# Kernel tuning notes

Measured on AMD Instinct MI355X. Metric: run time of the kernel, lower is better.

Reference implementation:

```python
import jax, jax.numpy as jnp
import numpy as np

B, N, OBS, H, S, A, K = 65536, 10, 64, 50, 10, 2, 2  # batch, agents, obs_dim, hidden, comm symbols, actions, k_steps
NEG = -1e9


def setup_inputs() -> dict:
    key = jax.random.key(0)
    ks = jax.random.split(key, 12)
    def lin(k, fan_in, shape):
        return (jax.random.uniform(k, shape, jnp.float32, -1.0, 1.0) / np.sqrt(fan_in).astype(np.float32))
    IN_F = H + S + H  # hidden + comm + skip(h0) = 110
    return {
        "obs": jax.random.normal(ks[0], (B, N, OBS), jnp.float32),
        "mask": jnp.ones((B, N), jnp.float32),
        "W_enc": lin(ks[1], OBS, (OBS, H)),
        "b_enc": lin(ks[2], OBS, (H,)),
        "W_f": lin(ks[3], IN_F, (K, IN_F, H)),
        "b_f": lin(ks[4], IN_F, (K, H)),
        "W_comm": lin(ks[5], H, (H, S)),
        "b_comm": lin(ks[6], H, (S,)),
        "W_pi": lin(ks[7], H, (H, A)),
        "b_pi": lin(ks[8], H, (A,)),
        "W_v": lin(ks[9], H, (H, 1)),
        "b_v": lin(ks[10], H, (1,)),
    }


def reference(obs, mask, W_enc, b_enc, W_f, b_f, W_comm, b_comm, W_pi, b_pi, W_v, b_v):
    mask3 = mask[..., None]                      # [B,N,1]
    h0 = jnp.tanh(obs @ W_enc + b_enc)           # [B,N,H]
    h = h0
    comm_logp = jnp.zeros(obs.shape[:2], obs.dtype)  # [B,N]
    c = jnp.zeros((*obs.shape[:2], S), obs.dtype)
    for i in range(K):  # k_steps is small & static
        comm_logits = h @ W_comm + b_comm        # [B,N,S]
        masked = jnp.where(mask3 == 0, NEG, comm_logits)
        logp = jax.nn.log_softmax(masked, axis=-1)
        w = jnp.argmax(masked, axis=-1)          # greedy symbol per agent [B,N]
        comm_logp = comm_logp + jnp.take_along_axis(logp, w[..., None], axis=-1)[..., 0] * mask
        w_onehot = jax.nn.one_hot(w, S, dtype=obs.dtype)  # [B,N,S]
        # bag-of-words OR aggregation across agents, broadcast back to every agent
        c = jnp.clip(jnp.sum(w_onehot, axis=1, keepdims=True), 0.0, 1.0)  # [B,1,S]
        c = jnp.broadcast_to(c, w_onehot.shape)  # [B,N,S]
        inp = jnp.concatenate([h, c, h0], axis=-1)  # [B,N,H+S+H]
        h = jnp.tanh(inp @ W_f[i] + b_f[i])
    logits = h @ W_pi + b_pi                      # [B,N,A]
    logits = jnp.where(mask3 == 0, NEG, logits)
    baseline = (h @ W_v + b_v)[..., 0] * mask     # [B,N]
    return logits, baseline, comm_logp, c
```

## Files before the change

### kernel.cpp

```cpp
#include <hip/hip_runtime.h>
#include <math.h>

#define NAGENT 10
#define OBS_D  64
#define HID    50
#define NSYM   10
#define NACT   2
#define KSTEPS 2
#define NEGV   (-1e9f)
#define INF    (HID + NSYM + HID)

#define BPB 6
#define TPB 64
#define AG  (BPB * NAGENT)

#define WENC_LD 52
#define WF_LD   52

#define SM_H1  (AG*51)
#define SM_C   (2*AG*51)
#define SM_TOT (SM_C + BPB*NSYM + 16)

__device__ __forceinline__ float fast_tanh(float x) {
  float xc = fminf(15.f, fmaxf(-15.f, x));
  float e  = __expf(2.f * xc);
  return __fdividef(e - 1.f, e + 1.f);
}

__global__ void prep_weights(const float* __restrict__ W_enc,
                             const float* __restrict__ W_f,
                             float* __restrict__ ws) {
  int i = blockIdx.x * blockDim.x + threadIdx.x;
  const int nEnc = OBS_D * WENC_LD;
  const int nF   = KSTEPS * INF * WF_LD;
  if (i < nEnc) {
    int k = i / WENC_LD, j = i % WENC_LD;
    ws[i] = (j < HID) ? W_enc[k*HID + j] : 0.f;
  } else if (i < nEnc + nF) {
    int r = i - nEnc;
    int s = r / (INF*WF_LD);
    int rem = r % (INF*WF_LD);
    int k = rem / WF_LD, j = rem % WF_LD;
    ws[i] = (j < HID) ? W_f[(s*INF + k)*HID + j] : 0.f;
  }
}

__global__ __launch_bounds__(TPB) void policy_kernel(
    const float* __restrict__ obs,
    const float* __restrict__ mask,
    const float* __restrict__ b_enc,
    const float* __restrict__ b_f,
    const float* __restrict__ W_comm,
    const float* __restrict__ b_comm,
    const float* __restrict__ W_pi,
    const float* __restrict__ b_pi,
    const float* __restrict__ W_v,
    const float* __restrict__ b_v,
    const float* __restrict__ W_encP,
    const float* __restrict__ W_fP,
    float* __restrict__ out,
    int B)
{
  __shared__ float smem[SM_TOT];
  const int t   = threadIdx.x;
  const int be0 = blockIdx.x * BPB;
  const int nbe = min(BPB, B - be0);
  const int nag = nbe * NAGENT;
  const int g0  = be0 * NAGENT;
  const bool act = (t < nag);
  const int ta  = act ? t : 0;
  const int bel = act ? (t / NAGENT) : 0;
  const long long g = (long long)g0 + t;
  const long long NA = (long long)B * NAGENT;

  {
    const float4* o4 = (const float4*)(obs + (long long)g0 * OBS_D);
    const int n4 = nag * (OBS_D/4);
    for (int idx = t; idx < n4; idx += TPB) {
      float4 v = o4[idx];
      int a = idx >> 4;
      int k = (idx & 15) << 2;
      float* p = &smem[a*65 + k];
      p[0]=v.x; p[1]=v.y; p[2]=v.z; p[3]=v.w;
    }
  }
  __syncthreads();

  float acc[HID];
  #pragma unroll
  for (int j=0;j<HID;j++) acc[j] = b_enc[j];
  {
    const int a65 = ta * 65;
    #pragma unroll 4
    for (int k=0;k<OBS_D;k++){
      float x = smem[a65 + k];
      const float* wr = &W_encP[k*WENC_LD];
      #pragma unroll
      for (int j=0;j<HID;j++) acc[j] = fmaf(x, wr[j], acc[j]);
    }
  }
  float hr[HID];
  #pragma unroll
  for (int j=0;j<HID;j++) hr[j] = fast_tanh(acc[j]);
  __syncthreads();
  if (act){
    #pragma unroll
    for (int j=0;j<HID;j++) smem[t*51 + j] = hr[j];
  }

  const float mk = act ? mask[g] : 1.f;
  float clp = 0.f;
  float c_reg[NSYM];

  #pragma unroll
  for (int i=0;i<KSTEPS;i++){
    float cl[NSYM];
    #pragma unroll
    for (int s=0;s<NSYM;s++) cl[s] = b_comm[s];
    #pragma unroll
    for (int k=0;k<HID;k++){
      #pragma unroll
      for (int s=0;s<NSYM;s++) cl[s] = fmaf(hr[k], W_comm[k*NSYM+s], cl[s]);
    }
    if (mk == 0.f){
      #pragma unroll
      for (int s=0;s<NSYM;s++) cl[s] = NEGV;
    }
    int w = 0; float best = cl[0];
    #pragma unroll
    for (int s=1;s<NSYM;s++){ if (cl[s] > best){ best = cl[s]; w = s; } }
    float se = 0.f;
    #pragma unroll
    for (int s=0;s<NSYM;s++) se += __expf(cl[s] - best);
    clp += (-__logf(se)) * mk;

    if (t < BPB*NSYM) smem[SM_C + t] = 0.f;
    __syncthreads();
    if (act) smem[SM_C + bel*NSYM + w] = 1.0f;
    __syncthreads();
    #pragma unroll
    for (int s=0;s<NSYM;s++) c_reg[s] = smem[SM_C + bel*NSYM + s];

    #pragma unroll
    for (int j=0;j<HID;j++) acc[j] = b_f[i*HID + j];
    #pragma unroll
    for (int s=0;s<NSYM;s++){
      const float cv = c_reg[s];
      const float* wr = &W_fP[(i*INF + HID + s)*WF_LD];
      #pragma unroll
      for (int j=0;j<HID;j++) acc[j] = fmaf(cv, wr[j], acc[j]);
    }
    const int a51 = ta*51;
    if (i == 0){
      #pragma unroll 2
      for (int k=0;k<HID;k++){
        float x = smem[a51 + k];
        const float* wa = &W_fP[(k)*WF_LD];
        const float* wd = &W_fP[(HID + NSYM + k)*WF_LD];
        #pragma unroll
        for (int j=0;j<HID;j++) acc[j] = fmaf(x, wa[j], acc[j]);
        #pragma unroll
        for (int j=0;j<HID;j++) acc[j] = fmaf(x, wd[j], acc[j]);
      }
    } else {
      #pragma unroll 2
      for (int k=0;k<HID;k++){
        float xa = smem[SM_H1 + a51 + k];
        float xd = smem[a51 + k];
        const float* wa = &W_fP[(INF + k)*WF_LD];
        const float* wd = &W_fP[(INF + HID + NSYM + k)*WF_LD];
        #pragma unroll
        for (int j=0;j<HID;j++) acc[j] = fmaf(xa, wa[j], acc[j]);
        #pragma unroll
        for (int j=0;j<HID;j++) acc[j] = fmaf(xd, wd[j], acc[j]);
      }
    }
    #pragma unroll
    for (int j=0;j<HID;j++) hr[j] = fast_tanh(acc[j]);
    if (i == 0){
      if (act){
        #pragma unroll
        for (int j=0;j<HID;j++) smem[SM_H1 + t*51 + j] = hr[j];
      }
    }
  }

  float l0 = b_pi[0], l1 = b_pi[1], bv = b_v[0];
  #pragma unroll
  for (int k=0;k<HID;k++){
    l0 = fmaf(hr[k], W_pi[k*NACT+0], l0);
    l1 = fmaf(hr[k], W_pi[k*NACT+1], l1);
    bv = fmaf(hr[k], W_v[k], bv);
  }
  if (act){
    const float lo0 = (mk==0.f) ? NEGV : l0;
    const float lo1 = (mk==0.f) ? NEGV : l1;
    out[g*2    ] = lo0;
    out[g*2 + 1] = lo1;
    out[NA*2 + g] = bv * mk;
    out[NA*3 + g] = clp;
    #pragma unroll
    for (int s=0;s<NSYM;s++) out[NA*4 + g*NSYM + s] = c_reg[s];
  }
}

extern "C" void kernel_launch(void* const* d_in, const int* in_sizes, int n_in,
                              void* d_out, int out_size, void* d_ws, size_t ws_size,
                              hipStream_t stream) {
  const float* obs    = (const float*)d_in[0];
  const float* mask   = (const float*)d_in[1];
  const float* W_enc  = (const float*)d_in[2];
  const float* b_enc  = (const float*)d_in[3];
  const float* W_f    = (const float*)d_in[4];
  const float* b_f    = (const float*)d_in[5];
  const float* W_comm = (const float*)d_in[6];
  const float* b_comm = (const float*)d_in[7];
  const float* W_pi   = (const float*)d_in[8];
  const float* b_pi   = (const float*)d_in[9];
  const float* W_v    = (const float*)d_in[10];
  const float* b_v    = (const float*)d_in[11];
  float* out = (float*)d_out;
  float* ws  = (float*)d_ws;

  const int B  = in_sizes[0] / (NAGENT * OBS_D);
  const int nP = OBS_D*WENC_LD + KSTEPS*INF*WF_LD;

  hipLaunchKernelGGL(prep_weights, dim3((nP + 255)/256), dim3(256), 0, stream,
                     W_enc, W_f, ws);

  const int grid = (B + BPB - 1) / BPB;
  hipLaunchKernelGGL(policy_kernel, dim3(grid), dim3(TPB), 0, stream,
                     obs, mask, b_enc, b_f, W_comm, b_comm, W_pi, b_pi, W_v, b_v,
                     ws, ws + OBS_D*WENC_LD, out, B);
}
```

Before: 614.7 us.

## Fold shared-input weights, replace LDS bag-of-words with ballot, stream obs directly

On step 0 h and h0 are the same vector, so the prep kernel sums their two weight blocks into one. The step-1 contribution of h0 is also computed during step 0, which lets the kernel read h0 only once. The OR aggregation across agents now uses wavefront ballots instead of shared-memory writes plus two barriers, and obs is read straight from global memory as float4 rather than staged through LDS. Outputs are written as float2, and a launch_bounds occupancy hint is added. In exchange, the pre1 accumulator array is kept live during step 0, which raises register pressure.

```diff
diff --git a/kernel.cpp b/kernel.cpp
--- a/kernel.cpp
+++ b/kernel.cpp
@@ -6,20 +6,20 @@
 #define HID    50
 #define NSYM   10
 #define NACT   2
-#define KSTEPS 2
 #define NEGV   (-1e9f)
-#define INF    (HID + NSYM + HID)
 
 #define BPB 6
 #define TPB 64
 #define AG  (BPB * NAGENT)
 
-#define WENC_LD 52
-#define WF_LD   52
-
-#define SM_H1  (AG*51)
-#define SM_C   (2*AG*51)
-#define SM_TOT (SM_C + BPB*NSYM + 16)
+#define LD 52
+
+#define OFF_WC0  3328
+#define OFF_W1S  5928
+#define OFF_W1H  8528
+#define OFF_WC0c 11128
+#define OFF_W1c  11648
+#define NPREP    (234 * LD)
 
 __device__ __forceinline__ float fast_tanh(float x) {
   float xc = fminf(15.f, fmaxf(-15.f, x));
@@ -31,21 +31,35 @@
                              const float* __restrict__ W_f,
                              float* __restrict__ ws) {
   int i = blockIdx.x * blockDim.x + threadIdx.x;
-  const int nEnc = OBS_D * WENC_LD;
-  const int nF   = KSTEPS * INF * WF_LD;
-  if (i < nEnc) {
-    int k = i / WENC_LD, j = i % WENC_LD;
-    ws[i] = (j < HID) ? W_enc[k*HID + j] : 0.f;
-  } else if (i < nEnc + nF) {
-    int r = i - nEnc;
-    int s = r / (INF*WF_LD);
-    int rem = r % (INF*WF_LD);
-    int k = rem / WF_LD, j = rem % WF_LD;
-    ws[i] = (j < HID) ? W_f[(s*INF + k)*HID + j] : 0.f;
-  }
-}
-
-__global__ __launch_bounds__(TPB) void policy_kernel(
+  if (i >= NPREP) return;
+  int j = i % LD;
+  int r = i / LD;
+  float v = 0.f;
+  if (j < HID) {
+    if      (r <  64)                { v = W_enc[r*HID + j]; }
+    else if (r < 114) { int k=r-64;    v = W_f[k*HID + j] + W_f[(60+k)*HID + j]; }
+    else if (r < 164) { int k=r-114;   v = W_f[(110+60+k)*HID + j]; }
+    else if (r < 214) { int k=r-164;   v = W_f[(110+k)*HID + j]; }
+    else if (r < 224) { int s=r-214;   v = W_f[(50+s)*HID + j]; }
+    else              { int s=r-224;   v = W_f[(110+50+s)*HID + j]; }
+  }
+  ws[i] = v;
+}
+
+__device__ __forceinline__ int comm_pick(float cl[NSYM], float mk, float& clp) {
+  #pragma unroll
+  for (int s = 0; s < NSYM; s++) cl[s] = (mk == 0.f) ? NEGV : cl[s];
+  int w = 0; float best = cl[0];
+  #pragma unroll
+  for (int s = 1; s < NSYM; s++) { bool b = cl[s] > best; best = b ? cl[s] : best; w = b ? s : w; }
+  float se = 0.f;
+  #pragma unroll
+  for (int s = 0; s < NSYM; s++) se += __expf(cl[s] - best);
+  clp += (-__logf(se)) * mk;
+  return w;
+}
+
+__global__ __launch_bounds__(TPB, 4) void policy_kernel(
     const float* __restrict__ obs,
     const float* __restrict__ mask,
     const float* __restrict__ b_enc,
@@ -56,151 +70,161 @@
     const float* __restrict__ b_pi,
     const float* __restrict__ W_v,
     const float* __restrict__ b_v,
-    const float* __restrict__ W_encP,
-    const float* __restrict__ W_fP,
+    const float* __restrict__ wsP,
     float* __restrict__ out,
     int B)
 {
-  __shared__ float smem[SM_TOT];
+  __shared__ float hbuf[AG * 51];
   const int t   = threadIdx.x;
   const int be0 = blockIdx.x * BPB;
   const int nbe = min(BPB, B - be0);
   const int nag = nbe * NAGENT;
-  const int g0  = be0 * NAGENT;
   const bool act = (t < nag);
-  const int ta  = act ? t : 0;
-  const int bel = act ? (t / NAGENT) : 0;
-  const long long g = (long long)g0 + t;
+  const int bel = t / NAGENT;
   const long long NA = (long long)B * NAGENT;
-
+  const long long g  = (long long)be0 * NAGENT + t;
+  const long long gc = act ? g : (NA - 1);
+  const int sl = act ? t : 0;
+
+  const float* WencP = wsP;
+  const float* WC0   = wsP + OFF_WC0;
+  const float* W1S   = wsP + OFF_W1S;
+  const float* W1H   = wsP + OFF_W1H;
+  const float* WC0c  = wsP + OFF_WC0c;
+  const float* W1c   = wsP + OFF_W1c;
+
+  const float mk = mask[gc];
+
+  float acc[HID];
+  #pragma unroll
+  for (int j = 0; j < HID; j++) acc[j] = b_enc[j];
   {
-    const float4* o4 = (const float4*)(obs + (long long)g0 * OBS_D);
-    const int n4 = nag * (OBS_D/4);
-    for (int idx = t; idx < n4; idx += TPB) {
-      float4 v = o4[idx];
-      int a = idx >> 4;
-      int k = (idx & 15) << 2;
-      float* p = &smem[a*65 + k];
-      p[0]=v.x; p[1]=v.y; p[2]=v.z; p[3]=v.w;
-    }
-  }
-  __syncthreads();
-
-  float acc[HID];
-  #pragma unroll
-  for (int j=0;j<HID;j++) acc[j] = b_enc[j];
+    const float4* o4 = (const float4*)(obs + gc * OBS_D);
+    #pragma unroll 2
+    for (int k4 = 0; k4 < OBS_D / 4; k4++) {
+      float4 v = o4[k4];
+      const float* wr = &WencP[k4 * 4 * LD];
+      #pragma unroll
+      for (int j = 0; j < HID; j++) acc[j] = fmaf(v.x, wr[j], acc[j]);
+      #pragma unroll
+      for (int j = 0; j < HID; j++) acc[j] = fmaf(v.y, wr[LD + j], acc[j]);
+      #pragma unroll
+      for (int j = 0; j < HID; j++) acc[j] = fmaf(v.z, wr[2 * LD + j], acc[j]);
+      #pragma unroll
+      for (int j = 0; j < HID; j++) acc[j] = fmaf(v.w, wr[3 * LD + j], acc[j]);
+    }
+  }
+
+  float cl[NSYM];
+  #pragma unroll
+  for (int s = 0; s < NSYM; s++) cl[s] = b_comm[s];
+  if (act) {
+    float* myh = &hbuf[t * 51];
+    #pragma unroll
+    for (int j = 0; j < HID; j++) {
+      float h = fast_tanh(acc[j]);
+      myh[j] = h;
+      const float* wc = &W_comm[j * NSYM];
+      #pragma unroll
+      for (int s = 0; s < NSYM; s++) cl[s] = fmaf(h, wc[s], cl[s]);
+    }
+  }
+
+  float clp = 0.f;
+
+  int w = comm_pick(cl, mk, clp);
+  const int sh = bel * NAGENT;
+  float c_reg[NSYM];
+  #pragma unroll
+  for (int s = 0; s < NSYM; s++) {
+    unsigned long long b = __ballot(w == s);
+    c_reg[s] = ((b >> sh) & 0x3FFULL) ? 1.f : 0.f;
+  }
+
+  float pre1[HID];
+  #pragma unroll
+  for (int j = 0; j < HID; j++) acc[j]  = b_f[j];
+  #pragma unroll
+  for (int j = 0; j < HID; j++) pre1[j] = b_f[HID + j];
   {
-    const int a65 = ta * 65;
-    #pragma unroll 4
-    for (int k=0;k<OBS_D;k++){
-      float x = smem[a65 + k];
-      const float* wr = &W_encP[k*WENC_LD];
-      #pragma unroll
-      for (int j=0;j<HID;j++) acc[j] = fmaf(x, wr[j], acc[j]);
-    }
-  }
-  float hr[HID];
-  #pragma unroll
-  for (int j=0;j<HID;j++) hr[j] = fast_tanh(acc[j]);
-  __syncthreads();
-  if (act){
-    #pragma unroll
-    for (int j=0;j<HID;j++) smem[t*51 + j] = hr[j];
-  }
-
-  const float mk = act ? mask[g] : 1.f;
-  float clp = 0.f;
-  float c_reg[NSYM];
-
-  #pragma unroll
-  for (int i=0;i<KSTEPS;i++){
-    float cl[NSYM];
-    #pragma unroll
-    for (int s=0;s<NSYM;s++) cl[s] = b_comm[s];
-    #pragma unroll
-    for (int k=0;k<HID;k++){
-      #pragma unroll
-      for (int s=0;s<NSYM;s++) cl[s] = fmaf(hr[k], W_comm[k*NSYM+s], cl[s]);
-    }
-    if (mk == 0.f){
-      #pragma unroll
-      for (int s=0;s<NSYM;s++) cl[s] = NEGV;
-    }
-    int w = 0; float best = cl[0];
-    #pragma unroll
-    for (int s=1;s<NSYM;s++){ if (cl[s] > best){ best = cl[s]; w = s; } }
-    float se = 0.f;
-    #pragma unroll
-    for (int s=0;s<NSYM;s++) se += __expf(cl[s] - best);
-    clp += (-__logf(se)) * mk;
-
-    if (t < BPB*NSYM) smem[SM_C + t] = 0.f;
-    __syncthreads();
-    if (act) smem[SM_C + bel*NSYM + w] = 1.0f;
-    __syncthreads();
-    #pragma unroll
-    for (int s=0;s<NSYM;s++) c_reg[s] = smem[SM_C + bel*NSYM + s];
-
-    #pragma unroll
-    for (int j=0;j<HID;j++) acc[j] = b_f[i*HID + j];
-    #pragma unroll
-    for (int s=0;s<NSYM;s++){
-      const float cv = c_reg[s];
-      const float* wr = &W_fP[(i*INF + HID + s)*WF_LD];
-      #pragma unroll
-      for (int j=0;j<HID;j++) acc[j] = fmaf(cv, wr[j], acc[j]);
-    }
-    const int a51 = ta*51;
-    if (i == 0){
-      #pragma unroll 2
-      for (int k=0;k<HID;k++){
-        float x = smem[a51 + k];
-        const float* wa = &W_fP[(k)*WF_LD];
-        const float* wd = &W_fP[(HID + NSYM + k)*WF_LD];
-        #pragma unroll
-        for (int j=0;j<HID;j++) acc[j] = fmaf(x, wa[j], acc[j]);
-        #pragma unroll
-        for (int j=0;j<HID;j++) acc[j] = fmaf(x, wd[j], acc[j]);
-      }
-    } else {
-      #pragma unroll 2
-      for (int k=0;k<HID;k++){
-        float xa = smem[SM_H1 + a51 + k];
-        float xd = smem[a51 + k];
-        const float* wa = &W_fP[(INF + k)*WF_LD];
-        const float* wd = &W_fP[(INF + HID + NSYM + k)*WF_LD];
-        #pragma unroll
-        for (int j=0;j<HID;j++) acc[j] = fmaf(xa, wa[j], acc[j]);
-        #pragma unroll
-        for (int j=0;j<HID;j++) acc[j] = fmaf(xd, wd[j], acc[j]);
-      }
-    }
-    #pragma unroll
-    for (int j=0;j<HID;j++) hr[j] = fast_tanh(acc[j]);
-    if (i == 0){
-      if (act){
-        #pragma unroll
-        for (int j=0;j<HID;j++) smem[SM_H1 + t*51 + j] = hr[j];
-      }
+    const float* myh = &hbuf[sl * 51];
+    #pragma unroll 2
+    for (int k = 0; k < HID; k++) {
+      float x = myh[k];
+      const float* w0 = &WC0[k * LD];
+      const float* w1 = &W1S[k * LD];
+      #pragma unroll
+      for (int j = 0; j < HID; j++) acc[j]  = fmaf(x, w0[j], acc[j]);
+      #pragma unroll
+      for (int j = 0; j < HID; j++) pre1[j] = fmaf(x, w1[j], pre1[j]);
+    }
+  }
+  #pragma unroll
+  for (int s = 0; s < NSYM; s++) {
+    float cv = c_reg[s];
+    const float* wr = &WC0c[s * LD];
+    #pragma unroll
+    for (int j = 0; j < HID; j++) acc[j] = fmaf(cv, wr[j], acc[j]);
+  }
+
+  #pragma unroll
+  for (int s = 0; s < NSYM; s++) cl[s] = b_comm[s];
+  if (act) {
+    float* myh = &hbuf[t * 51];
+    #pragma unroll
+    for (int j = 0; j < HID; j++) {
+      float h = fast_tanh(acc[j]);
+      myh[j] = h;
+      const float* wc = &W_comm[j * NSYM];
+      #pragma unroll
+      for (int s = 0; s < NSYM; s++) cl[s] = fmaf(h, wc[s], cl[s]);
+    }
+  }
+
+  w = comm_pick(cl, mk, clp);
+  #pragma unroll
+  for (int s = 0; s < NSYM; s++) {
+    unsigned long long b = __ballot(w == s);
+    c_reg[s] = ((b >> sh) & 0x3FFULL) ? 1.f : 0.f;
+  }
+
+  #pragma unroll
+  for (int s = 0; s < NSYM; s++) {
+    float cv = c_reg[s];
+    const float* wr = &W1c[s * LD];
+    #pragma unroll
+    for (int j = 0; j < HID; j++) pre1[j] = fmaf(cv, wr[j], pre1[j]);
+  }
+  {
+    const float* myh = &hbuf[sl * 51];
+    #pragma unroll 2
+    for (int k = 0; k < HID; k++) {
+      float x = myh[k];
+      const float* wr = &W1H[k * LD];
+      #pragma unroll
+      for (int j = 0; j < HID; j++) pre1[j] = fmaf(x, wr[j], pre1[j]);
     }
   }
 
   float l0 = b_pi[0], l1 = b_pi[1], bv = b_v[0];
   #pragma unroll
-  for (int k=0;k<HID;k++){
-    l0 = fmaf(hr[k], W_pi[k*NACT+0], l0);
-    l1 = fmaf(hr[k], W_pi[k*NACT+1], l1);
-    bv = fmaf(hr[k], W_v[k], bv);
-  }
-  if (act){
-    const float lo0 = (mk==0.f) ? NEGV : l0;
-    const float lo1 = (mk==0.f) ? NEGV : l1;
-    out[g*2    ] = lo0;
-    out[g*2 + 1] = lo1;
-    out[NA*2 + g] = bv * mk;
-    out[NA*3 + g] = clp;
-    #pragma unroll
-    for (int s=0;s<NSYM;s++) out[NA*4 + g*NSYM + s] = c_reg[s];
+  for (int j = 0; j < HID; j++) {
+    float h = fast_tanh(pre1[j]);
+    l0 = fmaf(h, W_pi[j * NACT + 0], l0);
+    l1 = fmaf(h, W_pi[j * NACT + 1], l1);
+    bv = fmaf(h, W_v[j], bv);
+  }
+
+  if (act) {
+    float2* o2 = (float2*)out;
+    o2[g] = make_float2((mk == 0.f) ? NEGV : l0, (mk == 0.f) ? NEGV : l1);
+    out[NA * 2 + g] = bv * mk;
+    out[NA * 3 + g] = clp;
+    float2* c2 = (float2*)(out + NA * 4);
+    const long long cb = g * (NSYM / 2);
+    #pragma unroll
+    for (int s = 0; s < NSYM / 2; s++)
+      c2[cb + s] = make_float2(c_reg[2 * s], c_reg[2 * s + 1]);
   }
 }
 
@@ -222,14 +246,13 @@
   float* out = (float*)d_out;
   float* ws  = (float*)d_ws;
 
-  const int B  = in_sizes[0] / (NAGENT * OBS_D);
-  const int nP = OBS_D*WENC_LD + KSTEPS*INF*WF_LD;
-
-  hipLaunchKernelGGL(prep_weights, dim3((nP + 255)/256), dim3(256), 0, stream,
+  const int B = in_sizes[0] / (NAGENT * OBS_D);
+
+  hipLaunchKernelGGL(prep_weights, dim3((NPREP + 255) / 256), dim3(256), 0, stream,
                      W_enc, W_f, ws);
 
   const int grid = (B + BPB - 1) / BPB;
   hipLaunchKernelGGL(policy_kernel, dim3(grid), dim3(TPB), 0, stream,
                      obs, mask, b_enc, b_f, W_comm, b_comm, W_pi, b_pi, W_v, b_v,
-                     ws, ws + OBS_D*WENC_LD, out, B);
-}
+                     ws, out, B);
+}
```

After: 535.1 us. 1.15x faster.
